# Kernel tuning notes

Measured on AMD Instinct MI355X. Metric: run time of the kernel, lower is better.

Reference implementation:

```python
import jax, jax.numpy as jnp
import numpy as np
from jax import lax

N, S, F_IN = 50000, 16, 64
HID, HEADS = 128, 4
C = HID // HEADS  # 32
E = 1600000
NEG_SLOPE = 0.2


def setup_inputs() -> dict:
    key = jax.random.key(0)
    ks = jax.random.split(key, 16)
    sc = lambda *sh: 1.0 / np.sqrt(sh[-1])
    inp = {}
    inp['node_features_sequence'] = jax.random.normal(ks[0], (N, S, F_IN), dtype=jnp.float32)
    inp['edge_index'] = jax.random.randint(ks[1], (2, E), 0, N, dtype=jnp.int64)
    # GRU params (single layer, order r,z,n as in torch)
    inp['gru_w_ih'] = jax.random.normal(ks[2], (3 * HID, F_IN), jnp.float32) * sc(F_IN)
    inp['gru_w_hh'] = jax.random.normal(ks[3], (3 * HID, HID), jnp.float32) * sc(HID)
    inp['gru_b_ih'] = jax.random.normal(ks[4], (3 * HID,), jnp.float32) * 0.01
    inp['gru_b_hh'] = jax.random.normal(ks[5], (3 * HID,), jnp.float32) * 0.01
    # GAT layer 1
    inp['gat1_w'] = jax.random.normal(ks[6], (HID, HID), jnp.float32) * sc(HID)
    inp['gat1_a_src'] = jax.random.normal(ks[7], (HEADS, C), jnp.float32) * sc(C)
    inp['gat1_a_dst'] = jax.random.normal(ks[8], (HEADS, C), jnp.float32) * sc(C)
    inp['gat1_b'] = jnp.zeros((HID,), jnp.float32)
    # GAT layer 2
    inp['gat2_w'] = jax.random.normal(ks[9], (HID, HID), jnp.float32) * sc(HID)
    inp['gat2_a_src'] = jax.random.normal(ks[10], (HEADS, C), jnp.float32) * sc(C)
    inp['gat2_a_dst'] = jax.random.normal(ks[11], (HEADS, C), jnp.float32) * sc(C)
    inp['gat2_b'] = jnp.zeros((HID,), jnp.float32)
    # classifier
    inp['clf_w'] = jax.random.normal(ks[12], (1, HID), jnp.float32) * sc(HID)
    inp['clf_b'] = jnp.zeros((1,), jnp.float32)
    return inp


def gru_last(xs, w_ih, w_hh, b_ih, b_hh):
    # xs: [N, S, F] -> last hidden [N, H]
    n, _, _ = xs.shape
    h_dim = w_hh.shape[1]
    gi_all = jnp.einsum('nsf,gf->nsg', xs, w_ih) + b_ih  # [N,S,3H]
    gi_all = jnp.swapaxes(gi_all, 0, 1)  # [S,N,3H]

    def step(h, gi):
        gh = h @ w_hh.T + b_hh
        i_r, i_z, i_n = jnp.split(gi, 3, axis=-1)
        h_r, h_z, h_n = jnp.split(gh, 3, axis=-1)
        r = jax.nn.sigmoid(i_r + h_r)
        z = jax.nn.sigmoid(i_z + h_z)
        nn_ = jnp.tanh(i_n + r * h_n)
        h_new = (1.0 - z) * nn_ + z * h
        return h_new, None

    h0 = jnp.zeros((n, h_dim), xs.dtype)
    h_last, _ = lax.scan(step, h0, gi_all)
    return h_last


def gat_layer(x, src, dst, w, a_src, a_dst, b):
    # x: [N, HID]; PyG GATConv with add_self_loops, concat heads
    n = x.shape[0]
    h = (x @ w.T).reshape(n, HEADS, C)  # [N,H,C]
    a_s = jnp.einsum('nhc,hc->nh', h, a_src)  # [N,H]
    a_d = jnp.einsum('nhc,hc->nh', h, a_dst)
    e = jax.nn.leaky_relu(a_s[src] + a_d[dst], NEG_SLOPE)  # [E',H]
    m = jax.ops.segment_max(e, dst, num_segments=n)
    m = jnp.where(jnp.isfinite(m), m, 0.0)
    ex = jnp.exp(e - m[dst])
    denom = jax.ops.segment_sum(ex, dst, num_segments=n)
    alpha = ex / (denom[dst] + 1e-16)  # [E',H]
    msg = h[src] * alpha[:, :, None]  # [E',H,C]
    out = jax.ops.segment_sum(msg, dst, num_segments=n)  # [N,H,C]
    return out.reshape(n, HEADS * C) + b


def reference(node_features_sequence, edge_index,
              gru_w_ih, gru_w_hh, gru_b_ih, gru_b_hh,
              gat1_w, gat1_a_src, gat1_a_dst, gat1_b,
              gat2_w, gat2_a_src, gat2_a_dst, gat2_b,
              clf_w, clf_b):
    n = node_features_sequence.shape[0]
    # add self loops once (same structure for both layers)
    loops = jnp.arange(n, dtype=edge_index.dtype)
    src = jnp.concatenate([edge_index[0], loops])
    dst = jnp.concatenate([edge_index[1], loops])

    x = gru_last(node_features_sequence, gru_w_ih, gru_w_hh, gru_b_ih, gru_b_hh)
    x = jax.nn.elu(gat_layer(x, src, dst, gat1_w, gat1_a_src, gat1_a_dst, gat1_b))
    x = jax.nn.elu(gat_layer(x, src, dst, gat2_w, gat2_a_src, gat2_a_dst, gat2_b))
    return jax.nn.sigmoid(x @ clf_w.T + clf_b)  # [N,1]
```

## Files before the change

kernel.cpp:

```cpp
#include <hip/hip_runtime.h>
#include <hip/hip_bf16.h>
#include <hip/hip_fp16.h>
#include <math.h>

#define N_NODES 50000
#define NP      50048
#define SEQ     16
#define FIN     64
#define HID     128
#define NEDGE   1600000
#define NB_SCAN 196
#define AGG_CAP 96

typedef __attribute__((ext_vector_type(8))) short short8;
typedef __attribute__((ext_vector_type(4))) float f32x4;

__device__ __forceinline__ float lrelu02(float v) { return v > 0.f ? v : 0.2f * v; }
__device__ __forceinline__ float frcp(float v) { return __builtin_amdgcn_rcpf(v); }
__device__ __forceinline__ float sigmoidf_(float v) { return frcp(1.f + __expf(-v)); }
__device__ __forceinline__ float eluf_(float v) { return v > 0.f ? v : (__expf(v) - 1.f); }

__device__ __forceinline__ unsigned bfpk(float lo, float hi) {
    union { __hip_bfloat162 h; unsigned u; } c;
    c.h = __float22bfloat162_rn(make_float2(lo, hi));
    return c.u;
}
__device__ __forceinline__ unsigned hfpk(float lo, float hi) {
    union { __half2 h; unsigned u; } c;
    c.h = __float22half2_rn(make_float2(lo, hi));
    return c.u;
}
__device__ __forceinline__ float2 h2f2(unsigned u) {
    union { unsigned u; __half2 h; } c;
    c.u = u;
    return __half22float2(c.h);
}
__device__ __forceinline__ short8 pack8(float4 a, float4 b) {
    union { short8 s; unsigned u[4]; } r;
    r.u[0] = bfpk(a.x, a.y); r.u[1] = bfpk(a.z, a.w);
    r.u[2] = bfpk(b.x, b.y); r.u[3] = bfpk(b.z, b.w);
    return r.s;
}

__global__ __launch_bounds__(512, 2) void gru_fused(
    const float* __restrict__ x,
    const float* __restrict__ w_ih,
    const float* __restrict__ w_hh,
    const float* __restrict__ b_ih,
    const float* __restrict__ b_hh,
    float* __restrict__ hout)
{
    __shared__ __align__(16) short hA[2][32][72];
    __shared__ __align__(16) short xB[2][32][72];

    const int tid  = threadIdx.x;
    const int wave = tid >> 6;
    const int lane = tid & 63;
    const int q    = lane >> 4;
    const int rl   = lane & 15;
    const int n0   = blockIdx.x * 32;
    const int ch   = wave * 16 + rl;

    short8 whhf[3][4];
    short8 wihf[3][2];
#pragma unroll
    for (int g = 0; g < 3; g++) {
        int row = g * 128 + ch;
#pragma unroll
        for (int kc = 0; kc < 4; kc++) {
            const float* p = w_hh + row * HID + kc * 32 + q * 8;
            whhf[g][kc] = pack8(*(const float4*)p, *(const float4*)(p + 4));
        }
#pragma unroll
        for (int kc = 0; kc < 2; kc++) {
            const float* p = w_ih + row * FIN + kc * 32 + q * 8;
            wihf[g][kc] = pack8(*(const float4*)p, *(const float4*)(p + 4));
        }
    }

    const float br  = b_ih[ch] + b_hh[ch];
    const float bz  = b_ih[128 + ch] + b_hh[128 + ch];
    const float bin = b_ih[256 + ch];
    const float bhn = b_hh[256 + ch];

    const int sn = tid >> 4;
    const int sk = (tid & 15) * 4;
    int sgn = n0 + sn; if (sgn > N_NODES - 1) sgn = N_NODES - 1;
    const float* xsp = x + (size_t)sgn * SEQ * FIN + sk;

    float hreg[2][4];
#pragma unroll
    for (int mt = 0; mt < 2; mt++)
#pragma unroll
        for (int r = 0; r < 4; r++) hreg[mt][r] = 0.f;

    {
        float4 v = *(const float4*)(xsp);
        int2 pv;
        pv.x = (int)bfpk(v.x, v.y);
        pv.y = (int)bfpk(v.z, v.w);
        *(int2*)&xB[0][sn][sk] = pv;
    }
    __syncthreads();

    for (int t = 0; t < SEQ; t++) {
        const int xb = t & 1;
        short8 xf[2][2], hf[2][4];
#pragma unroll
        for (int mt = 0; mt < 2; mt++)
#pragma unroll
            for (int kc = 0; kc < 2; kc++)
                xf[mt][kc] = *(const short8*)&xB[xb][mt * 16 + rl][kc * 32 + q * 8];
        if (t > 0) {
            const int hb = (t - 1) & 1;
#pragma unroll
            for (int mt = 0; mt < 2; mt++)
#pragma unroll
                for (int kc = 0; kc < 4; kc++)
                    hf[mt][kc] = *(const short8*)&hA[hb][mt * 16 + rl][kc * 32 + q * 8];
        }

        float4 xs;
        if (t + 1 < SEQ) xs = *(const float4*)(xsp + (t + 1) * FIN);

        f32x4 accr[2], accz[2], accin[2], acchn[2];
#pragma unroll
        for (int mt = 0; mt < 2; mt++) {
            accr[mt] = (f32x4)0.f; accz[mt] = (f32x4)0.f;
            accin[mt] = (f32x4)0.f; acchn[mt] = (f32x4)0.f;
#pragma unroll
            for (int kc = 0; kc < 2; kc++) {
                accr[mt]  = __builtin_amdgcn_mfma_f32_16x16x32_bf16(xf[mt][kc], wihf[0][kc], accr[mt], 0, 0, 0);
                accz[mt]  = __builtin_amdgcn_mfma_f32_16x16x32_bf16(xf[mt][kc], wihf[1][kc], accz[mt], 0, 0, 0);
                accin[mt] = __builtin_amdgcn_mfma_f32_16x16x32_bf16(xf[mt][kc], wihf[2][kc], accin[mt], 0, 0, 0);
            }
            if (t > 0) {
#pragma unroll
                for (int kc = 0; kc < 4; kc++) {
                    accr[mt]  = __builtin_amdgcn_mfma_f32_16x16x32_bf16(hf[mt][kc], whhf[0][kc], accr[mt], 0, 0, 0);
                    accz[mt]  = __builtin_amdgcn_mfma_f32_16x16x32_bf16(hf[mt][kc], whhf[1][kc], accz[mt], 0, 0, 0);
                    acchn[mt] = __builtin_amdgcn_mfma_f32_16x16x32_bf16(hf[mt][kc], whhf[2][kc], acchn[mt], 0, 0, 0);
                }
            }
        }

        if (t + 1 < SEQ) {
            int2 pv;
            pv.x = (int)bfpk(xs.x, xs.y);
            pv.y = (int)bfpk(xs.z, xs.w);
            *(int2*)&xB[(t + 1) & 1][sn][sk] = pv;
        }

        const int b = t & 1;
#pragma unroll
        for (int mt = 0; mt < 2; mt++) {
            float hv[4];
#pragma unroll
            for (int r = 0; r < 4; r++) {
                float rg = sigmoidf_(accr[mt][r] + br);
                float zg = sigmoidf_(accz[mt][r] + bz);
                float a  = accin[mt][r] + bin + rg * (acchn[mt][r] + bhn);
                float e  = __expf(2.f * a);
                float nn = 1.f - 2.f * frcp(e + 1.f);
                float h  = zg * (hreg[mt][r] - nn) + nn;
                hreg[mt][r] = h;
                hv[r] = h;
            }
            unsigned u01 = bfpk(hv[0], hv[1]);
            unsigned u23 = bfpk(hv[2], hv[3]);
            const int nb = mt * 16 + q * 4;
            hA[b][nb + 0][ch] = (short)(u01 & 0xFFFF);
            hA[b][nb + 1][ch] = (short)(u01 >> 16);
            hA[b][nb + 2][ch] = (short)(u23 & 0xFFFF);
            hA[b][nb + 3][ch] = (short)(u23 >> 16);
        }
        __syncthreads();
    }

#pragma unroll
    for (int mt = 0; mt < 2; mt++)
#pragma unroll
        for (int r = 0; r < 4; r++)
            hout[(size_t)(n0 + mt * 16 + q * 4 + r) * HID + ch] = hreg[mt][r];
}

__global__ void prep_weights(const float* __restrict__ g1w, const float* __restrict__ g2w,
                             float* __restrict__ g1T, float* __restrict__ g2T)
{
    int i = blockIdx.x * 256 + threadIdx.x;
    if (i < 128 * 128) {
        int k = i >> 7, g = i & 127;
        g1T[i] = g1w[g * 128 + k];
        g2T[i] = g2w[g * 128 + k];
    }
}

__global__ void count_edges(const int* __restrict__ dst, int* __restrict__ deg, int e)
{
    int i = blockIdx.x * 256 + threadIdx.x;
    if (i < e) atomicAdd(&deg[dst[i]], 1);
}

__device__ __forceinline__ int block_scan_inc(int v)
{
    int tid = threadIdx.x, lane = tid & 63, w = tid >> 6;
#pragma unroll
    for (int off = 1; off < 64; off <<= 1) {
        int tmp = __shfl_up(v, off, 64);
        if (lane >= off) v += tmp;
    }
    __shared__ int wsum[4];
    if (lane == 63) wsum[w] = v;
    __syncthreads();
    int add = 0;
    for (int i = 0; i < w; i++) add += wsum[i];
    return v + add;
}

__global__ void scan_block_sums(const int* __restrict__ deg, int* __restrict__ bsum, int n)
{
    int i = blockIdx.x * 256 + threadIdx.x;
    int v = (i < n) ? deg[i] : 0;
#pragma unroll
    for (int off = 32; off >= 1; off >>= 1) v += __shfl_xor(v, off, 64);
    __shared__ int ws[4];
    if ((threadIdx.x & 63) == 0) ws[threadIdx.x >> 6] = v;
    __syncthreads();
    if (threadIdx.x == 0) bsum[blockIdx.x] = ws[0] + ws[1] + ws[2] + ws[3];
}

__global__ void scan_bsum(int* __restrict__ bsum, int nb)
{
    int tid = threadIdx.x;
    int v = (tid < nb) ? bsum[tid] : 0;
    v = block_scan_inc(v);
    if (tid < nb) bsum[tid] = v;
}

__global__ void scan_final(const int* __restrict__ deg, const int* __restrict__ bsum,
                           int* __restrict__ rp, int n)
{
    int i = blockIdx.x * 256 + threadIdx.x;
    int v = (i < n) ? deg[i] : 0;
    int s = block_scan_inc(v);
    int add = (blockIdx.x > 0) ? bsum[blockIdx.x - 1] : 0;
    if (i < n) rp[i + 1] = s + add;
    if (i == 0) rp[0] = 0;
}

__global__ void fill_edges(const int* __restrict__ src, const int* __restrict__ dst,
                           const int* __restrict__ rp, int* __restrict__ cur,
                           int* __restrict__ col, int e)
{
    int i = blockIdx.x * 256 + threadIdx.x;
    if (i < e) {
        int d = dst[i];
        int pos = atomicAdd(&cur[d], 1);
        col[rp[d] + pos] = src[i];
    }
}

__global__ __launch_bounds__(256) void proj_attn(
    const float* __restrict__ x, const float* __restrict__ wT,
    const float* __restrict__ a_src, const float* __restrict__ a_dst,
    unsigned* __restrict__ hph, float* __restrict__ as_, float* __restrict__ ad_)
{
    __shared__ float xt[32][33];
    __shared__ float wt[32][128];
    __shared__ float ot[32][132];
    const int tid = threadIdx.x;
    const int tx = tid & 7;
    const int ty = tid >> 3;
    const int n0 = blockIdx.x * 32;
    float acc[4][4];
#pragma unroll
    for (int i = 0; i < 4; i++)
#pragma unroll
        for (int j = 0; j < 4; j++) acc[i][j] = 0.f;

    for (int k0 = 0; k0 < 128; k0 += 32) {
        __syncthreads();
#pragma unroll
        for (int i = 0; i < 4; i++) {
            int flat = tid + i * 256;
            int n = flat >> 5, k = flat & 31;
            xt[n][k] = x[(n0 + n) * HID + k0 + k];
        }
#pragma unroll
        for (int i = 0; i < 16; i++) {
            int flat = tid + i * 256;
            int kk = flat >> 7, g = flat & 127;
            wt[kk][g] = wT[(k0 + kk) * HID + g];
        }
        __syncthreads();
#pragma unroll 8
        for (int kk = 0; kk < 32; kk++) {
            float xv[4];
#pragma unroll
            for (int i = 0; i < 4; i++) xv[i] = xt[tx * 4 + i][kk];
            float4 wv = *(const float4*)&wt[kk][ty * 4];
#pragma unroll
            for (int i = 0; i < 4; i++) {
                acc[i][0] = fmaf(xv[i], wv.x, acc[i][0]);
                acc[i][1] = fmaf(xv[i], wv.y, acc[i][1]);
                acc[i][2] = fmaf(xv[i], wv.z, acc[i][2]);
                acc[i][3] = fmaf(xv[i], wv.w, acc[i][3]);
            }
        }
    }
#pragma unroll
    for (int i = 0; i < 4; i++) {
        int node = tx * 4 + i;
        ot[node][ty * 4 + 0] = acc[i][0];
        ot[node][ty * 4 + 1] = acc[i][1];
        ot[node][ty * 4 + 2] = acc[i][2];
        ot[node][ty * 4 + 3] = acc[i][3];
        uint2 pv;
        pv.x = hfpk(acc[i][0], acc[i][1]);
        pv.y = hfpk(acc[i][2], acc[i][3]);
        *(uint2*)&hph[(size_t)(n0 + node) * 64 + ty * 2] = pv;
    }
    __syncthreads();
    if (tid < 128) {
        int node = tid >> 2, head = tid & 3;
        const float* ar = a_src + head * 32;
        const float* br = a_dst + head * 32;
        float s = 0.f, d = 0.f;
#pragma unroll
        for (int j = 0; j < 32; j += 4) {
            float4 hv = *(const float4*)&ot[node][head * 32 + j];
            float4 av = *(const float4*)&ar[j];
            float4 bv = *(const float4*)&br[j];
            s += hv.x * av.x + hv.y * av.y + hv.z * av.z + hv.w * av.w;
            d += hv.x * bv.x + hv.y * bv.y + hv.z * bv.z + hv.w * bv.w;
        }
        as_[(n0 + node) * 4 + head] = s;
        ad_[(n0 + node) * 4 + head] = d;
    }
}

template <bool CLF>
__global__ __launch_bounds__(256) void gat_agg(
    const unsigned* __restrict__ hph, const float* __restrict__ as_,
    const float* __restrict__ ad_, const int* __restrict__ rp,
    const int* __restrict__ col, const float* __restrict__ bias,
    float* __restrict__ out, const float* __restrict__ cw,
    const float* __restrict__ cb, int n_nodes)
{
    __shared__ float exl[4][AGG_CAP][4];
    const int widx = threadIdx.x >> 6;
    const int lane = threadIdx.x & 63;
    const int n = blockIdx.x * 4 + widx;
    if (n >= n_nodes) return;

    const int e0 = rp[n], e1 = rp[n + 1];
    const int deg = e1 - e0;
    float4 adv = *(const float4*)&ad_[n * 4];
    float4 asn = *(const float4*)&as_[n * 4];
    float xs0 = __expf(lrelu02(asn.x + adv.x)), xs1 = __expf(lrelu02(asn.y + adv.y));
    float xs2 = __expf(lrelu02(asn.z + adv.z)), xs3 = __expf(lrelu02(asn.w + adv.w));

    float d0 = 0.f, d1 = 0.f, d2 = 0.f, d3 = 0.f;
    for (int e = e0 + lane; e < e1; e += 64) {
        int s = col[e];
        float4 a = *(const float4*)&as_[s * 4];
        float x0 = __expf(lrelu02(a.x + adv.x));
        float x1 = __expf(lrelu02(a.y + adv.y));
        float x2 = __expf(lrelu02(a.z + adv.z));
        float x3 = __expf(lrelu02(a.w + adv.w));
        int idx = e - e0;
        if (idx < AGG_CAP) {
            exl[widx][idx][0] = x0; exl[widx][idx][1] = x1;
            exl[widx][idx][2] = x2; exl[widx][idx][3] = x3;
        }
        d0 += x0; d1 += x1; d2 += x2; d3 += x3;
    }
#pragma unroll
    for (int off = 32; off >= 1; off >>= 1) {
        d0 += __shfl_xor(d0, off, 64);
        d1 += __shfl_xor(d1, off, 64);
        d2 += __shfl_xor(d2, off, 64);
        d3 += __shfl_xor(d3, off, 64);
    }
    d0 += xs0; d1 += xs1; d2 += xs2; d3 += xs3;
    float i0 = frcp(d0 + 1e-16f), i1 = frcp(d1 + 1e-16f);
    float i2 = frcp(d2 + 1e-16f), i3 = frcp(d3 + 1e-16f);

    const int head = lane >> 4;
    float invh = (head == 0) ? i0 : (head == 1) ? i1 : (head == 2) ? i2 : i3;
    float exsh = (head == 0) ? xs0 : (head == 1) ? xs1 : (head == 2) ? xs2 : xs3;
    float adh  = (head == 0) ? adv.x : (head == 1) ? adv.y : (head == 2) ? adv.z : adv.w;

    float2 sv = h2f2(hph[(size_t)n * 64 + lane]);
    float acc0 = exsh * sv.x;
    float acc1 = exsh * sv.y;

    if (deg <= AGG_CAP) {
        int e = e0;
        for (; e + 4 <= e1; e += 4) {
            int s_[4]; float w_[4]; unsigned u_[4];
#pragma unroll
            for (int u = 0; u < 4; u++) {
                s_[u] = col[e + u];
                w_[u] = exl[widx][e + u - e0][head];
            }
#pragma unroll
            for (int u = 0; u < 4; u++)
                u_[u] = hph[(size_t)s_[u] * 64 + lane];
#pragma unroll
            for (int u = 0; u < 4; u++) {
                float2 f = h2f2(u_[u]);
                acc0 = fmaf(w_[u], f.x, acc0);
                acc1 = fmaf(w_[u], f.y, acc1);
            }
        }
        for (; e < e1; e++) {
            int s = col[e];
            float w = exl[widx][e - e0][head];
            float2 f = h2f2(hph[(size_t)s * 64 + lane]);
            acc0 = fmaf(w, f.x, acc0);
            acc1 = fmaf(w, f.y, acc1);
        }
    } else {
        for (int e = e0; e < e1; e++) {
            int s = col[e];
            int idx = e - e0;
            float w;
            if (idx < AGG_CAP) w = exl[widx][idx][head];
            else               w = __expf(lrelu02(as_[s * 4 + head] + adh));
            float2 f = h2f2(hph[(size_t)s * 64 + lane]);
            acc0 = fmaf(w, f.x, acc0);
            acc1 = fmaf(w, f.y, acc1);
        }
    }

    float2 b2 = *(const float2*)&bias[2 * lane];
    float o0 = eluf_(acc0 * invh + b2.x);
    float o1 = eluf_(acc1 * invh + b2.y);
    if (CLF) {
        float2 cwv = *(const float2*)&cw[2 * lane];
        float v = o0 * cwv.x + o1 * cwv.y;
#pragma unroll
        for (int off = 32; off >= 1; off >>= 1) v += __shfl_xor(v, off, 64);
        if (lane == 0) out[n] = sigmoidf_(v + cb[0]);
    } else {
        *(float2*)&out[(size_t)n * HID + 2 * lane] = make_float2(o0, o1);
    }
}

extern "C" void kernel_launch(void* const* d_in, const int* in_sizes, int n_in,
                              void* d_out, int out_size, void* d_ws, size_t ws_size,
                              hipStream_t stream)
{
    const float* x     = (const float*)d_in[0];
    const int*   ei    = (const int*)d_in[1];
    const float* w_ih  = (const float*)d_in[2];
    const float* w_hh  = (const float*)d_in[3];
    const float* b_ih  = (const float*)d_in[4];
    const float* b_hh  = (const float*)d_in[5];
    const float* g1w   = (const float*)d_in[6];
    const float* g1as  = (const float*)d_in[7];
    const float* g1ad  = (const float*)d_in[8];
    const float* g1b   = (const float*)d_in[9];
    const float* g2w   = (const float*)d_in[10];
    const float* g2as  = (const float*)d_in[11];
    const float* g2ad  = (const float*)d_in[12];
    const float* g2b   = (const float*)d_in[13];
    const float* cw    = (const float*)d_in[14];
    const float* cb    = (const float*)d_in[15];
    float* out = (float*)d_out;

    char* wsb = (char*)d_ws;
    size_t off = 0;
    auto alc = [&](size_t bytes) { size_t o = off; off += (bytes + 255) & ~(size_t)255; return o; };

    float*    bufA = (float*)(wsb + alc((size_t)NP * HID * 4));
    float*    bufC = (float*)(wsb + alc((size_t)NP * HID * 4));
    unsigned* hph  = (unsigned*)(wsb + alc((size_t)NP * 64 * 4));
    float*    as_  = (float*)(wsb + alc((size_t)NP * 4 * 4));
    float*    ad_  = (float*)(wsb + alc((size_t)NP * 4 * 4));
    float*    g1T  = (float*)(wsb + alc((size_t)128 * 128 * 4));
    float*    g2T  = (float*)(wsb + alc((size_t)128 * 128 * 4));
    int*      rp   = (int*)(wsb + alc((size_t)(N_NODES + 1) * 4));
    int*      deg  = (int*)(wsb + alc((size_t)N_NODES * 4));
    int*      cur  = (int*)(wsb + alc((size_t)N_NODES * 4));
    int*      col  = (int*)(wsb + alc((size_t)NEDGE * 4));
    int*      bsum = (int*)(wsb + alc((size_t)256 * 4));

    const int* src = ei;
    const int* dst = ei + NEDGE;

    hipMemsetAsync(deg, 0, (size_t)N_NODES * 4, stream);
    hipMemsetAsync(cur, 0, (size_t)N_NODES * 4, stream);

    prep_weights<<<64, 256, 0, stream>>>(g1w, g2w, g1T, g2T);

    count_edges<<<NEDGE / 256, 256, 0, stream>>>(dst, deg, NEDGE);
    scan_block_sums<<<NB_SCAN, 256, 0, stream>>>(deg, bsum, N_NODES);
    scan_bsum<<<1, 256, 0, stream>>>(bsum, NB_SCAN);
    scan_final<<<NB_SCAN, 256, 0, stream>>>(deg, bsum, rp, N_NODES);
    fill_edges<<<NEDGE / 256, 256, 0, stream>>>(src, dst, rp, cur, col, NEDGE);

    gru_fused<<<NP / 32, 512, 0, stream>>>(x, w_ih, w_hh, b_ih, b_hh, bufA);

    proj_attn<<<NP / 32, 256, 0, stream>>>(bufA, g1T, g1as, g1ad, hph, as_, ad_);
    gat_agg<false><<<(N_NODES + 3) / 4, 256, 0, stream>>>(hph, as_, ad_, rp, col, g1b, bufC,
                                                          nullptr, nullptr, N_NODES);

    proj_attn<<<NP / 32, 256, 0, stream>>>(bufC, g2T, g2as, g2ad, hph, as_, ad_);
    gat_agg<true><<<(N_NODES + 3) / 4, 256, 0, stream>>>(hph, as_, ad_, rp, col, g2b, out,
                                                         cw, cb, N_NODES);
}
```

Baseline: 872.6 us.

## Fuse graph-build stages into GRU and projection kernels, single-pass GAT aggregation

Merges weight transpose and degree counting into the GRU launch, and the edge fill into the first projection launch, via block-index dispatch. It also replaces the three-kernel scan with one single-block scan and merges the two memsets into one. GAT aggregation drops its shared-memory staging pass and computes attention weights and the denominator in the same loop. GRU biases are folded into the MFMA accumulator init. Fewer launches and the overlap of irregular atomic work with compute trade against redundant exp computation and a serial scan.

```diff
diff --git a/kernel.cpp b/kernel.cpp
--- a/kernel.cpp
+++ b/kernel.cpp
@@ -9,8 +9,15 @@
 #define FIN     64
 #define HID     128
 #define NEDGE   1600000
-#define NB_SCAN 196
-#define AGG_CAP 96
+
+#define NB_PREP  32
+#define NB_COUNT 3125
+#define NB_GRU   (NP / 32)
+#define K1_GRID  (NB_PREP + NB_COUNT + NB_GRU)
+
+#define NB_PROJ  (NP / 32)
+#define NB_FILL  6250
+#define K3_GRID  (NB_PROJ + NB_FILL)
 
 typedef __attribute__((ext_vector_type(8))) short short8;
 typedef __attribute__((ext_vector_type(4))) float f32x4;
@@ -19,6 +26,7 @@
 __device__ __forceinline__ float frcp(float v) { return __builtin_amdgcn_rcpf(v); }
 __device__ __forceinline__ float sigmoidf_(float v) { return frcp(1.f + __expf(-v)); }
 __device__ __forceinline__ float eluf_(float v) { return v > 0.f ? v : (__expf(v) - 1.f); }
+__device__ __forceinline__ f32x4 mk4(float v) { f32x4 r; r[0] = v; r[1] = v; r[2] = v; r[3] = v; return r; }
 
 __device__ __forceinline__ unsigned bfpk(float lo, float hi) {
     union { __hip_bfloat162 h; unsigned u; } c;
@@ -42,13 +50,11 @@
     return r.s;
 }
 
-__global__ __launch_bounds__(512, 2) void gru_fused(
-    const float* __restrict__ x,
-    const float* __restrict__ w_ih,
-    const float* __restrict__ w_hh,
-    const float* __restrict__ b_ih,
-    const float* __restrict__ b_hh,
-    float* __restrict__ hout)
+__device__ void gru_body(
+    int bid,
+    const float* __restrict__ x, const float* __restrict__ w_ih,
+    const float* __restrict__ w_hh, const float* __restrict__ b_ih,
+    const float* __restrict__ b_hh, float* __restrict__ hout)
 {
     __shared__ __align__(16) short hA[2][32][72];
     __shared__ __align__(16) short xB[2][32][72];
@@ -58,7 +64,7 @@
     const int lane = tid & 63;
     const int q    = lane >> 4;
     const int rl   = lane & 15;
-    const int n0   = blockIdx.x * 32;
+    const int n0   = bid * 32;
     const int ch   = wave * 16 + rl;
 
     short8 whhf[3][4];
@@ -126,8 +132,8 @@
         f32x4 accr[2], accz[2], accin[2], acchn[2];
 #pragma unroll
         for (int mt = 0; mt < 2; mt++) {
-            accr[mt] = (f32x4)0.f; accz[mt] = (f32x4)0.f;
-            accin[mt] = (f32x4)0.f; acchn[mt] = (f32x4)0.f;
+            accr[mt] = mk4(br); accz[mt] = mk4(bz);
+            accin[mt] = mk4(bin); acchn[mt] = mk4(bhn);
 #pragma unroll
             for (int kc = 0; kc < 2; kc++) {
                 accr[mt]  = __builtin_amdgcn_mfma_f32_16x16x32_bf16(xf[mt][kc], wihf[0][kc], accr[mt], 0, 0, 0);
@@ -157,12 +163,12 @@
             float hv[4];
 #pragma unroll
             for (int r = 0; r < 4; r++) {
-                float rg = sigmoidf_(accr[mt][r] + br);
-                float zg = sigmoidf_(accz[mt][r] + bz);
-                float a  = accin[mt][r] + bin + rg * (acchn[mt][r] + bhn);
+                float rg = sigmoidf_(accr[mt][r]);
+                float zg = sigmoidf_(accz[mt][r]);
+                float a  = fmaf(rg, acchn[mt][r], accin[mt][r]);
                 float e  = __expf(2.f * a);
                 float nn = 1.f - 2.f * frcp(e + 1.f);
-                float h  = zg * (hreg[mt][r] - nn) + nn;
+                float h  = fmaf(zg, hreg[mt][r] - nn, nn);
                 hreg[mt][r] = h;
                 hv[r] = h;
             }
@@ -184,84 +190,66 @@
             hout[(size_t)(n0 + mt * 16 + q * 4 + r) * HID + ch] = hreg[mt][r];
 }
 
-__global__ void prep_weights(const float* __restrict__ g1w, const float* __restrict__ g2w,
-                             float* __restrict__ g1T, float* __restrict__ g2T)
-{
-    int i = blockIdx.x * 256 + threadIdx.x;
-    if (i < 128 * 128) {
+__global__ __launch_bounds__(512, 2) void k1_prep_count_gru(
+    const float* __restrict__ x, const float* __restrict__ w_ih,
+    const float* __restrict__ w_hh, const float* __restrict__ b_ih,
+    const float* __restrict__ b_hh, float* __restrict__ hout,
+    const float* __restrict__ g1w, const float* __restrict__ g2w,
+    float* __restrict__ g1T, float* __restrict__ g2T,
+    const int* __restrict__ dst, int* __restrict__ deg)
+{
+    const int gb = blockIdx.x;
+    if (gb < NB_PREP) {
+        int i = gb * 512 + threadIdx.x;
         int k = i >> 7, g = i & 127;
         g1T[i] = g1w[g * 128 + k];
         g2T[i] = g2w[g * 128 + k];
-    }
-}
-
-__global__ void count_edges(const int* __restrict__ dst, int* __restrict__ deg, int e)
-{
-    int i = blockIdx.x * 256 + threadIdx.x;
-    if (i < e) atomicAdd(&deg[dst[i]], 1);
-}
-
-__device__ __forceinline__ int block_scan_inc(int v)
-{
-    int tid = threadIdx.x, lane = tid & 63, w = tid >> 6;
-#pragma unroll
-    for (int off = 1; off < 64; off <<= 1) {
-        int tmp = __shfl_up(v, off, 64);
-        if (lane >= off) v += tmp;
-    }
-    __shared__ int wsum[4];
-    if (lane == 63) wsum[w] = v;
+        return;
+    }
+    if (gb < NB_PREP + NB_COUNT) {
+        int i = (gb - NB_PREP) * 512 + threadIdx.x;
+        if (i < NEDGE) atomicAdd(&deg[dst[i]], 1);
+        return;
+    }
+    gru_body(gb - NB_PREP - NB_COUNT, x, w_ih, w_hh, b_ih, b_hh, hout);
+}
+
+__global__ __launch_bounds__(1024) void scan_kernel(const int* __restrict__ deg,
+                                                    int* __restrict__ rp)
+{
+    __shared__ int ws[16];
+    __shared__ int carry;
+    const int tid = threadIdx.x, lane = tid & 63, w = tid >> 6;
+    if (tid == 0) { carry = 0; rp[0] = 0; }
     __syncthreads();
-    int add = 0;
-    for (int i = 0; i < w; i++) add += wsum[i];
-    return v + add;
-}
-
-__global__ void scan_block_sums(const int* __restrict__ deg, int* __restrict__ bsum, int n)
-{
-    int i = blockIdx.x * 256 + threadIdx.x;
-    int v = (i < n) ? deg[i] : 0;
-#pragma unroll
-    for (int off = 32; off >= 1; off >>= 1) v += __shfl_xor(v, off, 64);
-    __shared__ int ws[4];
-    if ((threadIdx.x & 63) == 0) ws[threadIdx.x >> 6] = v;
-    __syncthreads();
-    if (threadIdx.x == 0) bsum[blockIdx.x] = ws[0] + ws[1] + ws[2] + ws[3];
-}
-
-__global__ void scan_bsum(int* __restrict__ bsum, int nb)
-{
-    int tid = threadIdx.x;
-    int v = (tid < nb) ? bsum[tid] : 0;
-    v = block_scan_inc(v);
-    if (tid < nb) bsum[tid] = v;
-}
-
-__global__ void scan_final(const int* __restrict__ deg, const int* __restrict__ bsum,
-                           int* __restrict__ rp, int n)
-{
-    int i = blockIdx.x * 256 + threadIdx.x;
-    int v = (i < n) ? deg[i] : 0;
-    int s = block_scan_inc(v);
-    int add = (blockIdx.x > 0) ? bsum[blockIdx.x - 1] : 0;
-    if (i < n) rp[i + 1] = s + add;
-    if (i == 0) rp[0] = 0;
-}
-
-__global__ void fill_edges(const int* __restrict__ src, const int* __restrict__ dst,
-                           const int* __restrict__ rp, int* __restrict__ cur,
-                           int* __restrict__ col, int e)
-{
-    int i = blockIdx.x * 256 + threadIdx.x;
-    if (i < e) {
-        int d = dst[i];
-        int pos = atomicAdd(&cur[d], 1);
-        col[rp[d] + pos] = src[i];
-    }
-}
-
-__global__ __launch_bounds__(256) void proj_attn(
-    const float* __restrict__ x, const float* __restrict__ wT,
+    for (int base = 0; base < N_NODES; base += 1024) {
+        int i = base + tid;
+        int v = (i < N_NODES) ? deg[i] : 0;
+        int sv = v;
+#pragma unroll
+        for (int off = 1; off < 64; off <<= 1) {
+            int tmp = __shfl_up(sv, off, 64);
+            if (lane >= off) sv += tmp;
+        }
+        if (lane == 63) ws[w] = sv;
+        __syncthreads();
+        int add = 0, total = 0;
+#pragma unroll
+        for (int k = 0; k < 16; k++) {
+            int s = ws[k];
+            if (k < w) add += s;
+            total += s;
+        }
+        int incl = sv + add + carry;
+        if (i < N_NODES) rp[i + 1] = incl;
+        __syncthreads();
+        if (tid == 0) carry += total;
+        __syncthreads();
+    }
+}
+
+__device__ void proj_attn_body(
+    int bid, const float* __restrict__ x, const float* __restrict__ wT,
     const float* __restrict__ a_src, const float* __restrict__ a_dst,
     unsigned* __restrict__ hph, float* __restrict__ as_, float* __restrict__ ad_)
 {
@@ -271,7 +259,7 @@
     const int tid = threadIdx.x;
     const int tx = tid & 7;
     const int ty = tid >> 3;
-    const int n0 = blockIdx.x * 32;
+    const int n0 = bid * 32;
     float acc[4][4];
 #pragma unroll
     for (int i = 0; i < 4; i++)
@@ -339,6 +327,34 @@
     }
 }
 
+__global__ __launch_bounds__(256) void k3_proj_fill(
+    const float* __restrict__ xin, const float* __restrict__ wT,
+    const float* __restrict__ a_src, const float* __restrict__ a_dst,
+    unsigned* __restrict__ hph, float* __restrict__ as_, float* __restrict__ ad_,
+    const int* __restrict__ src, const int* __restrict__ dst,
+    const int* __restrict__ rp, int* __restrict__ cur, int* __restrict__ col)
+{
+    const int gb = blockIdx.x;
+    if (gb < NB_PROJ) {
+        proj_attn_body(gb, xin, wT, a_src, a_dst, hph, as_, ad_);
+        return;
+    }
+    int i = (gb - NB_PROJ) * 256 + threadIdx.x;
+    if (i < NEDGE) {
+        int d = dst[i];
+        int pos = atomicAdd(&cur[d], 1);
+        col[rp[d] + pos] = src[i];
+    }
+}
+
+__global__ __launch_bounds__(256) void proj_attn_kernel(
+    const float* __restrict__ xin, const float* __restrict__ wT,
+    const float* __restrict__ a_src, const float* __restrict__ a_dst,
+    unsigned* __restrict__ hph, float* __restrict__ as_, float* __restrict__ ad_)
+{
+    proj_attn_body(blockIdx.x, xin, wT, a_src, a_dst, hph, as_, ad_);
+}
+
 template <bool CLF>
 __global__ __launch_bounds__(256) void gat_agg(
     const unsigned* __restrict__ hph, const float* __restrict__ as_,
@@ -347,96 +363,53 @@
     float* __restrict__ out, const float* __restrict__ cw,
     const float* __restrict__ cb, int n_nodes)
 {
-    __shared__ float exl[4][AGG_CAP][4];
-    const int widx = threadIdx.x >> 6;
     const int lane = threadIdx.x & 63;
-    const int n = blockIdx.x * 4 + widx;
+    const int n = blockIdx.x * 4 + (threadIdx.x >> 6);
     if (n >= n_nodes) return;
 
     const int e0 = rp[n], e1 = rp[n + 1];
-    const int deg = e1 - e0;
+    const int head = lane >> 4;
     float4 adv = *(const float4*)&ad_[n * 4];
-    float4 asn = *(const float4*)&as_[n * 4];
-    float xs0 = __expf(lrelu02(asn.x + adv.x)), xs1 = __expf(lrelu02(asn.y + adv.y));
-    float xs2 = __expf(lrelu02(asn.z + adv.z)), xs3 = __expf(lrelu02(asn.w + adv.w));
-
-    float d0 = 0.f, d1 = 0.f, d2 = 0.f, d3 = 0.f;
-    for (int e = e0 + lane; e < e1; e += 64) {
-        int s = col[e];
-        float4 a = *(const float4*)&as_[s * 4];
-        float x0 = __expf(lrelu02(a.x + adv.x));
-        float x1 = __expf(lrelu02(a.y + adv.y));
-        float x2 = __expf(lrelu02(a.z + adv.z));
-        float x3 = __expf(lrelu02(a.w + adv.w));
-        int idx = e - e0;
-        if (idx < AGG_CAP) {
-            exl[widx][idx][0] = x0; exl[widx][idx][1] = x1;
-            exl[widx][idx][2] = x2; exl[widx][idx][3] = x3;
-        }
-        d0 += x0; d1 += x1; d2 += x2; d3 += x3;
-    }
-#pragma unroll
-    for (int off = 32; off >= 1; off >>= 1) {
-        d0 += __shfl_xor(d0, off, 64);
-        d1 += __shfl_xor(d1, off, 64);
-        d2 += __shfl_xor(d2, off, 64);
-        d3 += __shfl_xor(d3, off, 64);
-    }
-    d0 += xs0; d1 += xs1; d2 += xs2; d3 += xs3;
-    float i0 = frcp(d0 + 1e-16f), i1 = frcp(d1 + 1e-16f);
-    float i2 = frcp(d2 + 1e-16f), i3 = frcp(d3 + 1e-16f);
-
-    const int head = lane >> 4;
-    float invh = (head == 0) ? i0 : (head == 1) ? i1 : (head == 2) ? i2 : i3;
-    float exsh = (head == 0) ? xs0 : (head == 1) ? xs1 : (head == 2) ? xs2 : xs3;
-    float adh  = (head == 0) ? adv.x : (head == 1) ? adv.y : (head == 2) ? adv.z : adv.w;
-
+    float adh = (head == 0) ? adv.x : (head == 1) ? adv.y : (head == 2) ? adv.z : adv.w;
+
+    float ws = __expf(lrelu02(as_[n * 4 + head] + adh));
     float2 sv = h2f2(hph[(size_t)n * 64 + lane]);
-    float acc0 = exsh * sv.x;
-    float acc1 = exsh * sv.y;
-
-    if (deg <= AGG_CAP) {
-        int e = e0;
-        for (; e + 4 <= e1; e += 4) {
-            int s_[4]; float w_[4]; unsigned u_[4];
-#pragma unroll
-            for (int u = 0; u < 4; u++) {
-                s_[u] = col[e + u];
-                w_[u] = exl[widx][e + u - e0][head];
-            }
-#pragma unroll
-            for (int u = 0; u < 4; u++)
-                u_[u] = hph[(size_t)s_[u] * 64 + lane];
-#pragma unroll
-            for (int u = 0; u < 4; u++) {
-                float2 f = h2f2(u_[u]);
-                acc0 = fmaf(w_[u], f.x, acc0);
-                acc1 = fmaf(w_[u], f.y, acc1);
-            }
-        }
-        for (; e < e1; e++) {
-            int s = col[e];
-            float w = exl[widx][e - e0][head];
-            float2 f = h2f2(hph[(size_t)s * 64 + lane]);
+    float den = ws;
+    float acc0 = ws * sv.x;
+    float acc1 = ws * sv.y;
+
+    int e = e0;
+    for (; e + 4 <= e1; e += 4) {
+        int s_[4]; float a_[4]; unsigned u_[4];
+#pragma unroll
+        for (int u = 0; u < 4; u++) s_[u] = col[e + u];
+#pragma unroll
+        for (int u = 0; u < 4; u++) {
+            a_[u] = as_[s_[u] * 4 + head];
+            u_[u] = hph[(size_t)s_[u] * 64 + lane];
+        }
+#pragma unroll
+        for (int u = 0; u < 4; u++) {
+            float w = __expf(lrelu02(a_[u] + adh));
+            float2 f = h2f2(u_[u]);
+            den += w;
             acc0 = fmaf(w, f.x, acc0);
             acc1 = fmaf(w, f.y, acc1);
         }
-    } else {
-        for (int e = e0; e < e1; e++) {
-            int s = col[e];
-            int idx = e - e0;
-            float w;
-            if (idx < AGG_CAP) w = exl[widx][idx][head];
-            else               w = __expf(lrelu02(as_[s * 4 + head] + adh));
-            float2 f = h2f2(hph[(size_t)s * 64 + lane]);
-            acc0 = fmaf(w, f.x, acc0);
-            acc1 = fmaf(w, f.y, acc1);
-        }
-    }
-
+    }
+    for (; e < e1; e++) {
+        int s = col[e];
+        float w = __expf(lrelu02(as_[s * 4 + head] + adh));
+        float2 f = h2f2(hph[(size_t)s * 64 + lane]);
+        den += w;
+        acc0 = fmaf(w, f.x, acc0);
+        acc1 = fmaf(w, f.y, acc1);
+    }
+
+    float inv = frcp(den + 1e-16f);
     float2 b2 = *(const float2*)&bias[2 * lane];
-    float o0 = eluf_(acc0 * invh + b2.x);
-    float o1 = eluf_(acc1 * invh + b2.y);
+    float o0 = eluf_(acc0 * inv + b2.x);
+    float o1 = eluf_(acc1 * inv + b2.y);
     if (CLF) {
         float2 cwv = *(const float2*)&cw[2 * lane];
         float v = o0 * cwv.x + o1 * cwv.y;
@@ -482,32 +455,30 @@
     float*    g1T  = (float*)(wsb + alc((size_t)128 * 128 * 4));
     float*    g2T  = (float*)(wsb + alc((size_t)128 * 128 * 4));
     int*      rp   = (int*)(wsb + alc((size_t)(N_NODES + 1) * 4));
-    int*      deg  = (int*)(wsb + alc((size_t)N_NODES * 4));
-    int*      cur  = (int*)(wsb + alc((size_t)N_NODES * 4));
+    size_t    degoff = alc((size_t)N_NODES * 4);
+    int*      deg  = (int*)(wsb + degoff);
+    size_t    curoff = alc((size_t)N_NODES * 4);
+    int*      cur  = (int*)(wsb + curoff);
     int*      col  = (int*)(wsb + alc((size_t)NEDGE * 4));
-    int*      bsum = (int*)(wsb + alc((size_t)256 * 4));
 
     const int* src = ei;
     const int* dst = ei + NEDGE;
 
-    hipMemsetAsync(deg, 0, (size_t)N_NODES * 4, stream);
-    hipMemsetAsync(cur, 0, (size_t)N_NODES * 4, stream);
-
-    prep_weights<<<64, 256, 0, stream>>>(g1w, g2w, g1T, g2T);
-
-    count_edges<<<NEDGE / 256, 256, 0, stream>>>(dst, deg, NEDGE);
-    scan_block_sums<<<NB_SCAN, 256, 0, stream>>>(deg, bsum, N_NODES);
-    scan_bsum<<<1, 256, 0, stream>>>(bsum, NB_SCAN);
-    scan_final<<<NB_SCAN, 256, 0, stream>>>(deg, bsum, rp, N_NODES);
-    fill_edges<<<NEDGE / 256, 256, 0, stream>>>(src, dst, rp, cur, col, NEDGE);
-
-    gru_fused<<<NP / 32, 512, 0, stream>>>(x, w_ih, w_hh, b_ih, b_hh, bufA);
-
-    proj_attn<<<NP / 32, 256, 0, stream>>>(bufA, g1T, g1as, g1ad, hph, as_, ad_);
+    hipMemsetAsync(deg, 0, curoff + (size_t)N_NODES * 4 - degoff, stream);
+
+    k1_prep_count_gru<<<K1_GRID, 512, 0, stream>>>(
+        x, w_ih, w_hh, b_ih, b_hh, bufA, g1w, g2w, g1T, g2T, dst, deg);
+
+    scan_kernel<<<1, 1024, 0, stream>>>(deg, rp);
+
+    k3_proj_fill<<<K3_GRID, 256, 0, stream>>>(
+        bufA, g1T, g1as, g1ad, hph, as_, ad_, src, dst, rp, cur, col);
+
     gat_agg<false><<<(N_NODES + 3) / 4, 256, 0, stream>>>(hph, as_, ad_, rp, col, g1b, bufC,
                                                           nullptr, nullptr, N_NODES);
 
-    proj_attn<<<NP / 32, 256, 0, stream>>>(bufC, g2T, g2as, g2ad, hph, as_, ad_);
+    proj_attn_kernel<<<NB_PROJ, 256, 0, stream>>>(bufC, g2T, g2as, g2ad, hph, as_, ad_);
+
     gat_agg<true><<<(N_NODES + 3) / 4, 256, 0, stream>>>(hph, as_, ad_, rp, col, g2b, out,
                                                          cw, cb, N_NODES);
 }
```

Result: slower. 921.4 us (+5.6%).
